# Performance work log

Measured on AMD Instinct MI355X. Metric: run time of the kernel, lower is better.

The kernel has to match this reference:

```python
import jax, jax.numpy as jnp
import numpy as np

N_NODES = 25000
N_EDGES = 400000
IN_FEATS = 256
HIDDEN = 64
HEADS = 8
CLASSES = 32


def setup_inputs() -> dict:
    key = jax.random.key(0)
    ks = jax.random.split(key, 12)
    h = jax.random.normal(ks[0], (N_NODES, IN_FEATS), dtype=jnp.float32)
    src = jax.random.randint(ks[1], (N_EDGES,), 0, N_NODES, dtype=jnp.int32)
    dst = jnp.sort(jax.random.randint(ks[2], (N_EDGES,), 0, N_NODES, dtype=jnp.int32))
    s = 0.05  # param scale
    W1 = jax.random.normal(ks[3], (HIDDEN * HEADS, IN_FEATS), dtype=jnp.float32) * s
    al1 = jax.random.normal(ks[4], (1, HEADS, HIDDEN), dtype=jnp.float32) * s
    ar1 = jax.random.normal(ks[5], (1, HEADS, HIDDEN), dtype=jnp.float32) * s
    W2 = jax.random.normal(ks[6], (HIDDEN * HEADS, HIDDEN * HEADS), dtype=jnp.float32) * s
    al2 = jax.random.normal(ks[7], (1, HEADS, HIDDEN), dtype=jnp.float32) * s
    ar2 = jax.random.normal(ks[8], (1, HEADS, HIDDEN), dtype=jnp.float32) * s
    W3 = jax.random.normal(ks[9], (CLASSES, HIDDEN * HEADS), dtype=jnp.float32) * s
    al3 = jax.random.normal(ks[10], (1, 1, CLASSES), dtype=jnp.float32) * s
    ar3 = jax.random.normal(ks[11], (1, 1, CLASSES), dtype=jnp.float32) * s
    return dict(h=h, src=src, dst=dst, W1=W1, al1=al1, ar1=ar1,
                W2=W2, al2=al2, ar2=ar2, W3=W3, al3=al3, ar3=ar3)


def gat_layer(x, src, dst, W, al, ar, use_elu):
    # x: [N, Din]; W: [H*F, Din]; al/ar: [1, H, F]
    n = x.shape[0]
    H, F = al.shape[1], al.shape[2]
    z = (x @ W.T).reshape(n, H, F)                      # [N,H,F]
    el = jnp.sum(z * al, axis=-1)                       # [N,H]
    er = jnp.sum(z * ar, axis=-1)                       # [N,H]
    e = jax.nn.leaky_relu(el[src] + er[dst], 0.2)       # [E,H]
    # segment softmax over incoming edges of each dst node
    m = jax.ops.segment_max(e, dst, num_segments=n, indices_are_sorted=True)   # [N,H]
    ex = jnp.exp(e - m[dst])                            # [E,H]
    den = jax.ops.segment_sum(ex, dst, num_segments=n, indices_are_sorted=True)  # [N,H]
    alpha = ex / den[dst]                               # [E,H]
    out = jax.ops.segment_sum(alpha[:, :, None] * z[src], dst,
                              num_segments=n, indices_are_sorted=True)  # [N,H,F]
    if use_elu:
        out = jax.nn.elu(out)
    return out.reshape(n, H * F)


def reference(h, src, dst, W1, al1, ar1, W2, al2, ar2, W3, al3, ar3):
    x = gat_layer(h, src, dst, W1, al1, ar1, True)
    x = gat_layer(x, src, dst, W2, al2, ar2, True)
    x = gat_layer(x, src, dst, W3, al3, ar3, False)
    return x
```

## Files before the change

kernel.cpp:

```cpp
#include <hip/hip_runtime.h>
#include <cstdint>

#define DEVINL __device__ __forceinline__

typedef uint16_t u16;
typedef uint32_t u32;
typedef uint64_t u64;
typedef __attribute__((ext_vector_type(8))) short short8;
typedef __attribute__((ext_vector_type(4))) float floatx4;
typedef __attribute__((ext_vector_type(4))) u32 u32x4;
typedef const __attribute__((address_space(1))) void* gas_ptr;
typedef __attribute__((address_space(3))) void* las_ptr;

DEVINL u16 f2bf(float f) {
  u32 u = __float_as_uint(f);
  u32 r = u + 0x7FFFu + ((u >> 16) & 1u);
  return (u16)(r >> 16);
}
DEVINL float bf2f(u16 b) { return __uint_as_float((u32)b << 16); }
DEVINL float bf_lo(u32 u) { return __uint_as_float(u << 16); }
DEVINL float bf_hi(u32 u) { return __uint_as_float(u & 0xFFFF0000u); }


__global__ __launch_bounds__(256)
void prep_kernel(const int* __restrict__ dst, int* __restrict__ rs,
                 const float* __restrict__ h, u16* __restrict__ A1,
                 const float* __restrict__ W1, const float* __restrict__ W2,
                 const float* __restrict__ W3, u16* __restrict__ B1,
                 u16* __restrict__ B2, u16* __restrict__ B3,
                 int N, int E, int Mpad)
{
  const int b = blockIdx.x, tid = threadIdx.x;
  if (b < 25000) {
    int idx = b * 256 + tid;
    int m = idx >> 8, k = idx & 255;
    float a = h[idx];
    u16 hi = f2bf(a);
    u16 lo = f2bf(a - bf2f(hi));
    size_t cs = (size_t)Mpad * 64;
    size_t pos = (size_t)m * 64 + (k & 63);
    A1[(size_t)(k >> 6) * cs + pos] = hi;
    A1[(size_t)((k >> 6) + 4) * cs + pos] = lo;
    return;
  }
  if (b < 26600) {
    int idx = (b - 25000) * 256 + tid;
    if (idx < 512 * 256) {
      int m = idx >> 8, k = idx & 255;
      u16 hh = f2bf(W1[idx]);
      size_t cs = 512 * 64;
      size_t pos = (size_t)m * 64 + (k & 63);
      B1[(size_t)(k >> 6) * cs + pos] = hh;
      B1[(size_t)((k >> 6) + 4) * cs + pos] = hh;
      return;
    }
    idx -= 512 * 256;
    if (idx < 512 * 512) {
      int m = idx >> 9, k = idx & 511;
      u16 hh = f2bf(W2[idx]);
      size_t cs = 512 * 64;
      size_t pos = (size_t)m * 64 + (k & 63);
      B2[(size_t)(k >> 6) * cs + pos] = hh;
      B2[(size_t)((k >> 6) + 8) * cs + pos] = hh;
      return;
    }
    idx -= 512 * 512;
    {
      int m = idx >> 9, k = idx & 511;
      u16 hh = f2bf(W3[idx]);
      size_t cs = 32 * 64;
      size_t pos = (size_t)m * 64 + (k & 63);
      B3[(size_t)(k >> 6) * cs + pos] = hh;
      B3[(size_t)((k >> 6) + 8) * cs + pos] = hh;
      return;
    }
  }
  {
    int n = (b - 26600) * 256 + tid;
    if (n > N) return;
    int lo = 0, hi = E;
    while (lo < hi) { int mid = (lo + hi) >> 1; if (dst[mid] < n) lo = mid + 1; else hi = mid; }
    rs[n] = lo;
  }
}

template<int BN, int OUTM>
__global__ __launch_bounds__(512)
void gemm_bt_kernel(const u16* __restrict__ A, const u16* __restrict__ B,
                    float* __restrict__ Cf, u16* __restrict__ Cb,
                    const float* __restrict__ al, const float* __restrict__ ar,
                    float* __restrict__ el, float* __restrict__ er,
                    int M, int Nout, int Mpad, int kcLen)
{
  constexpr int BM = 128, CF = BN / 16;
  constexpr int BCALLS_B = (BN * 64) / 512;
  __shared__ __align__(16) u16 As[2][BM * 64];
  __shared__ __align__(16) u16 Bs[2][BN * 64];
  const int tid  = threadIdx.x;
  const int wave = tid >> 6;
  const int lane = tid & 63;
  const int quad = lane >> 4;
  const int l16  = lane & 15;
  const int lrow = lane >> 3;
  const int lq   = lane & 7;

  int bx, by;
  if (OUTM == 1) {
    int bid = blockIdx.x;
    int nY = (M + 127) >> 7;
    int fullG = nY >> 3;
    if ((bid >> 5) < fullG) {
      int rem = bid & 31;
      by = ((bid >> 5) << 3) + (rem & 7);
      bx = rem >> 3;
    } else {
      int t = bid - (fullG << 5);
      int tailY = nY - (fullG << 3);
      by = (fullG << 3) + t % tailY;
      bx = t / tailY;
    }
  } else { bx = blockIdx.x; by = blockIdx.y; }

  const int rowBase = by * BM;
  const int colBase = (OUTM == 2) ? 0 : bx * BN;
  const int kcStart = 0;

  floatx4 acc[CF];
  #pragma unroll
  for (int c = 0; c < CF; ++c)
    acc[c] = (floatx4){0.f, 0.f, 0.f, 0.f};

  const size_t aCS = (size_t)Mpad * 64;
  const size_t bCS = (size_t)Nout * 64;
  const u16* aTile = A + (size_t)rowBase * 64;
  const u16* bTile = B + (size_t)colBase * 64;

  auto stage = [&](int buf, int kc) {
    const u16* aB = aTile + (size_t)kc * aCS;
    #pragma unroll
    for (int i = 0; i < 2; ++i) {
      int c = wave + 8 * i;
      int row = c * 8 + lrow;
      const u16* gp = aB + row * 64 + ((lq ^ (row & 7)) << 3);
      __builtin_amdgcn_global_load_lds((gas_ptr)gp, (las_ptr)(&As[buf][c * 512]), 16, 0, 0);
    }
    const u16* bB = bTile + (size_t)kc * bCS;
    #pragma unroll
    for (int i = 0; i < (BCALLS_B + 7) / 8; ++i) {
      int c = wave + 8 * i;
      if (c < BCALLS_B) {
        int row = c * 8 + lrow;
        const u16* gp = bB + row * 64 + ((lq ^ (row & 7)) << 3);
        __builtin_amdgcn_global_load_lds((gas_ptr)gp, (las_ptr)(&Bs[buf][c * 512]), 16, 0, 0);
      }
    }
  };

  stage(0, kcStart);
  int cur = 0;
  for (int t = 0; t < kcLen; ++t) {
    __syncthreads();
    if (t + 1 < kcLen) stage(cur ^ 1, kcStart + t + 1);
    const u16* Asb = &As[cur][0];
    const u16* Bsb = &Bs[cur][0];
    const int r0 = 16 * wave + l16;
    #pragma unroll
    for (int kk = 0; kk < 2; ++kk) {
      short8 a0 = *(const short8*)(Asb + r0 * 64 + ((((kk << 2) + quad) ^ (r0 & 7)) << 3));
      #pragma unroll
      for (int c = 0; c < CF; ++c) {
        int rb = 16 * c + l16;
        short8 b = *(const short8*)(Bsb + rb * 64 + ((((kk << 2) + quad) ^ (rb & 7)) << 3));
        acc[c] = __builtin_amdgcn_mfma_f32_16x16x32_bf16(a0, b, acc[c], 0, 0, 0);
      }
    }
    cur ^= 1;
  }

  #pragma unroll
  for (int c = 0; c < CF; ++c)
    #pragma unroll
    for (int i = 0; i < 4; ++i) {
      int gr = rowBase + 16 * wave + quad * 4 + i;
      if (gr < M) {
        int gc = colBase + 16 * c + l16;
        if (OUTM == 1) Cb[(size_t)gr * Nout + gc] = f2bf(acc[c][i]);
        else           Cf[(size_t)gr * Nout + gc] = acc[c][i];
      }
    }

  if (OUTM == 1) {
    #pragma unroll
    for (int i = 0; i < 4; ++i) {
      int gr = rowBase + 16 * wave + quad * 4 + i;
      #pragma unroll
      for (int hp = 0; hp < 2; ++hp) {
        float sl = 0.f, sr = 0.f;
        #pragma unroll
        for (int cc = 0; cc < 4; ++cc) {
          int c = hp * 4 + cc;
          int gc = colBase + 16 * c + l16;
          float zv = acc[c][i];
          sl += zv * al[gc];
          sr += zv * ar[gc];
        }
        #pragma unroll
        for (int m = 1; m < 16; m <<= 1) {
          sl += __shfl_xor(sl, m, 64);
          sr += __shfl_xor(sr, m, 64);
        }
        if (l16 == 0 && gr < M) {
          int hh = colBase / 64 + hp;
          el[(size_t)gr * 8 + hh] = sl;
          er[(size_t)gr * 8 + hh] = sr;
        }
      }
    }
  } else {
    #pragma unroll
    for (int i = 0; i < 4; ++i) {
      int gr = rowBase + 16 * wave + quad * 4 + i;
      float sl = 0.f, sr = 0.f;
      #pragma unroll
      for (int c = 0; c < CF; ++c) {
        int gc = 16 * c + l16;
        float zv = acc[c][i];
        sl += zv * al[gc];
        sr += zv * ar[gc];
      }
      #pragma unroll
      for (int m = 1; m < 16; m <<= 1) {
        sl += __shfl_xor(sl, m, 64);
        sr += __shfl_xor(sr, m, 64);
      }
      if (l16 == 0 && gr < M) {
        el[gr] = sl;
        er[gr] = sr;
      }
    }
  }
}

__global__ __launch_bounds__(64)
void agg_bf16_kernel(const u16* __restrict__ z, const float* __restrict__ el,
                     const float* __restrict__ er, const int* __restrict__ src,
                     const int* __restrict__ rs, u16* __restrict__ a2out, int Mpad)
{
  const int n = blockIdx.x, tid = threadIdx.x;
  const int s = rs[n], e = rs[n + 1];
  const int c0 = tid * 8;
  const int h = tid >> 3;
  const float er_h = er[(size_t)n * 8 + h];

  float acc[8];
  #pragma unroll
  for (int j = 0; j < 8; ++j) acc[j] = 0.f;
  float den = 0.f;

  for (int k0 = s; k0 < e; k0 += 8) {
    const int kc = e - k0;
    #pragma unroll
    for (int kk = 0; kk < 8; ++kk) {
      if (kk < kc) {
        int si = src[k0 + kk];
        float v = el[(size_t)si * 8 + h] + er_h;
        v = (v > 0.f) ? v : 0.2f * v;
        float wgt = __expf(v);
        u32x4 zz = *(const u32x4*)(z + (size_t)si * 512 + c0);
        #pragma unroll
        for (int j = 0; j < 4; ++j) {
          acc[2 * j]     += wgt * bf_lo(zz[j]);
          acc[2 * j + 1] += wgt * bf_hi(zz[j]);
        }
        den += wgt;
      }
    }
  }

  const float r = (e > s) ? (1.f / den) : 0.f;
  u32x4 hp, lp;
  #pragma unroll
  for (int j = 0; j < 4; ++j) {
    float o0 = acc[2 * j] * r, o1 = acc[2 * j + 1] * r;
    o0 = (o0 > 0.f) ? o0 : (__expf(o0) - 1.f);
    o1 = (o1 > 0.f) ? o1 : (__expf(o1) - 1.f);
    u16 h0 = f2bf(o0), h1 = f2bf(o1);
    u16 l0 = f2bf(o0 - bf2f(h0)), l1 = f2bf(o1 - bf2f(h1));
    hp[j] = ((u32)h1 << 16) | h0;
    lp[j] = ((u32)l1 << 16) | l0;
  }
  const int ck = tid >> 3;
  const int ko = (tid & 7) << 3;
  const size_t cs = (size_t)Mpad * 64;
  u16* p = a2out + (size_t)n * 64 + ko;
  *(u32x4*)(p + (size_t)ck * cs) = hp;
  *(u32x4*)(p + (size_t)(ck + 8) * cs) = lp;
}

__global__ __launch_bounds__(64)
void agg3_kernel(const float* __restrict__ z, const float* __restrict__ el,
                 const float* __restrict__ er, const int* __restrict__ src,
                 const int* __restrict__ rs, float* __restrict__ out)
{
  const int n = blockIdx.x, tid = threadIdx.x;
  const int s = rs[n], e = rs[n + 1];
  const bool active = (tid < 32);
  const float er_n = er[n];
  float acc = 0.f, den = 0.f;

  for (int k0 = s; k0 < e; k0 += 8) {
    const int kc = e - k0;
    #pragma unroll
    for (int kk = 0; kk < 8; ++kk) {
      if (kk < kc) {
        int si = src[k0 + kk];
        float v = el[si] + er_n;
        v = (v > 0.f) ? v : 0.2f * v;
        float wgt = __expf(v);
        if (active) acc += wgt * z[(size_t)si * 32 + tid];
        den += wgt;
      }
    }
  }
  if (active) out[(size_t)n * 32 + tid] = (e > s) ? (acc / den) : 0.f;
}

extern "C" void kernel_launch(void* const* d_in, const int* in_sizes, int n_in,
                              void* d_out, int out_size, void* d_ws, size_t ws_size,
                              hipStream_t stream)
{
  constexpr int N = 25000, E = 400000, K1 = 256, HF = 512, CLS = 32;
  constexpr int Mpad = 25088;
  const float* h   = (const float*)d_in[0];
  const int*   src = (const int*)d_in[1];
  const int*   dst = (const int*)d_in[2];
  const float* W1  = (const float*)d_in[3];
  const float* al1 = (const float*)d_in[4];
  const float* ar1 = (const float*)d_in[5];
  const float* W2  = (const float*)d_in[6];
  const float* al2 = (const float*)d_in[7];
  const float* ar2 = (const float*)d_in[8];
  const float* W3  = (const float*)d_in[9];
  const float* al3 = (const float*)d_in[10];
  const float* ar3 = (const float*)d_in[11];
  float* out = (float*)d_out;

  char* w = (char*)d_ws;
  auto take = [&](size_t bytes) {
    char* p = w;
    w += (bytes + 255) & ~(size_t)255;
    return p;
  };
  int*   rs  = (int*)  take((size_t)(N + 1) * sizeof(int));
  float* el  = (float*)take((size_t)N * 8 * sizeof(float));
  float* er  = (float*)take((size_t)N * 8 * sizeof(float));
  float* z3  = (float*)take((size_t)N * CLS * sizeof(float));
  u16*   zb  = (u16*)  take((size_t)N * HF * sizeof(u16));
  u16*   A2  = (u16*)  take((size_t)16 * Mpad * 64 * sizeof(u16));
  u16*   B1  = (u16*)  take((size_t)8  * HF * 64 * sizeof(u16));
  u16*   B2  = (u16*)  take((size_t)16 * HF * 64 * sizeof(u16));
  u16*   B3  = (u16*)  take((size_t)16 * CLS * 64 * sizeof(u16));
  u16*   A1  = A2;

  prep_kernel<<<dim3(25000 + 1600 + 98), 256, 0, stream>>>(
      dst, rs, h, A1, W1, W2, W3, B1, B2, B3, N, E, Mpad);

  const int gemmBlocks = 4 * (Mpad / 128);

  gemm_bt_kernel<128, 1><<<dim3(gemmBlocks), 512, 0, stream>>>(A1, B1, nullptr, zb,
      al1, ar1, el, er, N, HF, Mpad, 8);
  agg_bf16_kernel<<<dim3(N), 64, 0, stream>>>(zb, el, er, src, rs, A2, Mpad);

  gemm_bt_kernel<128, 1><<<dim3(gemmBlocks), 512, 0, stream>>>(A2, B2, nullptr, zb,
      al2, ar2, el, er, N, HF, Mpad, 16);
  agg_bf16_kernel<<<dim3(N), 64, 0, stream>>>(zb, el, er, src, rs, A2, Mpad);

  gemm_bt_kernel<32, 2><<<dim3(1, Mpad / 128), 512, 0, stream>>>(A2, B3, z3, nullptr,
      al3, ar3, el, er, N, CLS, Mpad, 16);
  agg3_kernel<<<dim3(N), 64, 0, stream>>>(z3, el, er, src, rs, out);
}
```

Before: 353.5 us.

## Split aggregation by head slice with persistent grid-stride blocks

The bf16 aggregation kernel now launches a fixed grid of 8 head slices times 2048 slots. Each 64-lane block handles one head's 64 columns and strides over nodes, instead of one block covering all 512 columns of a node with 8 columns per lane. The aim is a wavefront count independent of N and per-head parallelism with coalesced 2-byte loads. In exchange, each lane issues scalar 16-bit gathers instead of 16-byte vector loads, and the src and el reads are repeated eight times, once per slice.

After: 569.3 us. 1.61x slower.

```diff
diff --git a/kernel.cpp b/kernel.cpp
--- a/kernel.cpp
+++ b/kernel.cpp
@@ -244,57 +244,46 @@
 __global__ __launch_bounds__(64)
 void agg_bf16_kernel(const u16* __restrict__ z, const float* __restrict__ el,
                      const float* __restrict__ er, const int* __restrict__ src,
-                     const int* __restrict__ rs, u16* __restrict__ a2out, int Mpad)
-{
-  const int n = blockIdx.x, tid = threadIdx.x;
-  const int s = rs[n], e = rs[n + 1];
-  const int c0 = tid * 8;
-  const int h = tid >> 3;
-  const float er_h = er[(size_t)n * 8 + h];
-
-  float acc[8];
-  #pragma unroll
-  for (int j = 0; j < 8; ++j) acc[j] = 0.f;
-  float den = 0.f;
-
-  for (int k0 = s; k0 < e; k0 += 8) {
-    const int kc = e - k0;
-    #pragma unroll
-    for (int kk = 0; kk < 8; ++kk) {
-      if (kk < kc) {
-        int si = src[k0 + kk];
-        float v = el[(size_t)si * 8 + h] + er_h;
-        v = (v > 0.f) ? v : 0.2f * v;
-        float wgt = __expf(v);
-        u32x4 zz = *(const u32x4*)(z + (size_t)si * 512 + c0);
-        #pragma unroll
-        for (int j = 0; j < 4; ++j) {
-          acc[2 * j]     += wgt * bf_lo(zz[j]);
-          acc[2 * j + 1] += wgt * bf_hi(zz[j]);
+                     const int* __restrict__ rs, u16* __restrict__ a2out,
+                     int Mpad, int N, int slots)
+{
+  const int bid = blockIdx.x;
+  const int slice = bid & 7;
+  const int bslot = bid >> 3;
+  const int lane = threadIdx.x;
+  const int c = slice * 64 + lane;
+  const size_t cs = (size_t)Mpad * 64;
+  const u16* zc = z + c;
+
+  for (int n = bslot; n < N; n += slots) {
+    const int s = rs[n], e = rs[n + 1];
+    const float er_h = er[(size_t)n * 8 + slice];
+    float acc = 0.f, den = 0.f;
+
+    for (int k0 = s; k0 < e; k0 += 8) {
+      const int kc = e - k0;
+      #pragma unroll
+      for (int kk = 0; kk < 8; ++kk) {
+        if (kk < kc) {
+          int si = src[k0 + kk];
+          float v = el[(size_t)si * 8 + slice] + er_h;
+          v = (v > 0.f) ? v : 0.2f * v;
+          float wgt = __expf(v);
+          float zv = bf2f(zc[(size_t)si * 512]);
+          acc += wgt * zv;
+          den += wgt;
         }
-        den += wgt;
-      }
-    }
-  }
-
-  const float r = (e > s) ? (1.f / den) : 0.f;
-  u32x4 hp, lp;
-  #pragma unroll
-  for (int j = 0; j < 4; ++j) {
-    float o0 = acc[2 * j] * r, o1 = acc[2 * j + 1] * r;
-    o0 = (o0 > 0.f) ? o0 : (__expf(o0) - 1.f);
-    o1 = (o1 > 0.f) ? o1 : (__expf(o1) - 1.f);
-    u16 h0 = f2bf(o0), h1 = f2bf(o1);
-    u16 l0 = f2bf(o0 - bf2f(h0)), l1 = f2bf(o1 - bf2f(h1));
-    hp[j] = ((u32)h1 << 16) | h0;
-    lp[j] = ((u32)l1 << 16) | l0;
-  }
-  const int ck = tid >> 3;
-  const int ko = (tid & 7) << 3;
-  const size_t cs = (size_t)Mpad * 64;
-  u16* p = a2out + (size_t)n * 64 + ko;
-  *(u32x4*)(p + (size_t)ck * cs) = hp;
-  *(u32x4*)(p + (size_t)(ck + 8) * cs) = lp;
+      }
+    }
+
+    const float r = (e > s) ? (1.f / den) : 0.f;
+    float o = acc * r;
+    o = (o > 0.f) ? o : (__expf(o) - 1.f);
+    u16 hi = f2bf(o);
+    u16 lo = f2bf(o - bf2f(hi));
+    a2out[(size_t)slice * cs + (size_t)n * 64 + lane] = hi;
+    a2out[(size_t)(slice + 8) * cs + (size_t)n * 64 + lane] = lo;
+  }
 }
 
 __global__ __launch_bounds__(64)
@@ -331,6 +320,7 @@
 {
   constexpr int N = 25000, E = 400000, K1 = 256, HF = 512, CLS = 32;
   constexpr int Mpad = 25088;
+  constexpr int AGG_SLOTS = 2048;
   const float* h   = (const float*)d_in[0];
   const int*   src = (const int*)d_in[1];
   const int*   dst = (const int*)d_in[2];
@@ -366,14 +356,17 @@
       dst, rs, h, A1, W1, W2, W3, B1, B2, B3, N, E, Mpad);
 
   const int gemmBlocks = 4 * (Mpad / 128);
+  const int aggBlocks  = 8 * AGG_SLOTS;
 
   gemm_bt_kernel<128, 1><<<dim3(gemmBlocks), 512, 0, stream>>>(A1, B1, nullptr, zb,
       al1, ar1, el, er, N, HF, Mpad, 8);
-  agg_bf16_kernel<<<dim3(N), 64, 0, stream>>>(zb, el, er, src, rs, A2, Mpad);
+  agg_bf16_kernel<<<dim3(aggBlocks), 64, 0, stream>>>(zb, el, er, src, rs, A2,
+      Mpad, N, AGG_SLOTS);
 
   gemm_bt_kernel<128, 1><<<dim3(gemmBlocks), 512, 0, stream>>>(A2, B2, nullptr, zb,
       al2, ar2, el, er, N, HF, Mpad, 16);
-  agg_bf16_kernel<<<dim3(N), 64, 0, stream>>>(zb, el, er, src, rs, A2, Mpad);
+  agg_bf16_kernel<<<dim3(aggBlocks), 64, 0, stream>>>(zb, el, er, src, rs, A2,
+      Mpad, N, AGG_SLOTS);
 
   gemm_bt_kernel<32, 2><<<dim3(1, Mpad / 128), 512, 0, stream>>>(A2, B3, z3, nullptr,
       al3, ar3, el, er, N, CLS, Mpad, 16);
```
